# Kernel optimization log

Measured on AMD Instinct MI355X. Metric: run time of the kernel, lower is better.

Reference implementation:

```python
import jax, jax.numpy as jnp
import numpy as np

B, T, N, V, D = 2048, 50, 100, 50000, 512  # batch, targets/ex, noises/ex (=2*T), vocab, label_size


def setup_inputs() -> dict:
    key = jax.random.key(0)
    k1, k2, k3, k4 = jax.random.split(key, 4)
    features = jax.random.normal(k1, (B, D), dtype=jnp.float32)
    targets = jax.random.randint(k2, (B, T), 0, V, dtype=jnp.int64)
    noises = jax.random.randint(k3, (B, N), 0, V, dtype=jnp.int64)
    W = jax.random.normal(k4, (V, D), dtype=jnp.float32) * 0.02  # h2o.weight [V, D]
    return {"features": features, "targets": targets, "noises": noises, "W": W}


def reference(features, targets, noises, W):
    # Per example: out = concat([W[targets] @ f, -(W[noises] @ f)]);
    # loss_i = -mean(logsigmoid(out)); total = sum_i loss_i. (dropout=0 / eval)
    pos = jnp.einsum('btd,bd->bt', W[targets], features)   # [B, T]
    neg = jnp.einsum('bnd,bd->bn', W[noises], features)    # [B, N]
    ls = jax.nn.log_sigmoid
    per_ex = -(jnp.sum(ls(pos), axis=1) + jnp.sum(ls(-neg), axis=1)) / (T + N)
    return jnp.sum(per_ex)
```

## Files before the change

kernel.cpp:

```cpp
#include <hip/hip_runtime.h>
#include <math.h>

constexpr int B_ = 2048;
constexpr int T_ = 50;
constexpr int N_ = 100;
constexpr int D_ = 512;
constexpr int NTOT = T_ + N_;

__global__ __launch_bounds__(256, 8) void nsl_kernel(
    const float* __restrict__ features,
    const int* __restrict__ targets,
    const int* __restrict__ noises,
    const float* __restrict__ W,
    float* __restrict__ out)
{
    const int b    = blockIdx.x;
    const int tid  = threadIdx.x;
    const int lane = tid & 63;
    const int wave = tid >> 6;

    __shared__ int   s_idx[NTOT];
    __shared__ float s_wsum[4];

    if (tid < T_)          s_idx[tid] = targets[(size_t)b * T_ + tid];
    else if (tid < NTOT)   s_idx[tid] = noises[(size_t)b * N_ + (tid - T_)];
    __syncthreads();

    const float4* f4 = reinterpret_cast<const float4*>(features + (size_t)b * D_);
    const float4 fa = f4[lane];
    const float4 fb = f4[lane + 64];

    float acc = 0.f;

    for (int t = wave; t < NTOT; t += 4) {
        const int idx = s_idx[t];
        const float4* w4 = reinterpret_cast<const float4*>(W + (size_t)idx * D_);
        const float4 wa = w4[lane];
        const float4 wb = w4[lane + 64];

        float p = wa.x * fa.x + wa.y * fa.y + wa.z * fa.z + wa.w * fa.w
                + wb.x * fb.x + wb.y * fb.y + wb.z * fb.z + wb.w * fb.w;

        #pragma unroll
        for (int s = 32; s >= 1; s >>= 1)
            p += __shfl_xor(p, s, 64);

        const float x = (t < T_) ? p : -p;
        const float ls = fminf(x, 0.f) - log1pf(__expf(-fabsf(x)));
        acc += ls;
    }

    if (lane == 0) s_wsum[wave] = acc;
    __syncthreads();

    if (tid == 0) {
        const float s = s_wsum[0] + s_wsum[1] + s_wsum[2] + s_wsum[3];
        atomicAdd(out, -s / (float)NTOT);
    }
}

extern "C" void kernel_launch(void* const* d_in, const int* in_sizes, int n_in,
                              void* d_out, int out_size, void* d_ws, size_t ws_size,
                              hipStream_t stream) {
    const float* features = (const float*)d_in[0];
    const int*   targets  = (const int*)d_in[1];
    const int*   noises   = (const int*)d_in[2];
    const float* W        = (const float*)d_in[3];
    float*       out      = (float*)d_out;

    hipMemsetAsync(out, 0, sizeof(float), stream);

    nsl_kernel<<<B_, 256, 0, stream>>>(features, targets, noises, W, out);
}
```

Before: 226.8 us.

## Gather eight rows per wave iteration with transposed butterfly shuffle reduction

Each wave now issues loads for eight gathered W rows per iteration instead of one, which keeps more memory requests in flight for this bandwidth-bound gather. The per-row full wave reductions are replaced by a transposed butterfly that reduces eight partial dot products together, cutting shuffle count. Each result ends up replicated across eight lanes, so the final sum is divided by eight to compensate. The index list is padded to 152 entries, and the padded rows load row 0 and are masked out. The log1p call is replaced by the faster __logf, which gives up a little accuracy. Holding eight rows at once raises register pressure.

Result: no change. 224.1 us (-1.2%).

```diff
diff --git a/kernel.cpp b/kernel.cpp
--- a/kernel.cpp
+++ b/kernel.cpp
@@ -1,11 +1,13 @@
 #include <hip/hip_runtime.h>
 #include <math.h>
 
-constexpr int B_ = 2048;
-constexpr int T_ = 50;
-constexpr int N_ = 100;
-constexpr int D_ = 512;
+constexpr int B_   = 2048;
+constexpr int T_   = 50;
+constexpr int N_   = 100;
+constexpr int D_   = 512;
 constexpr int NTOT = T_ + N_;
+constexpr int NPAD = 152;
+constexpr int NCHK = NPAD / 8;
 
 __global__ __launch_bounds__(256, 8) void nsl_kernel(
     const float* __restrict__ features,
@@ -19,11 +21,12 @@
     const int lane = tid & 63;
     const int wave = tid >> 6;
 
-    __shared__ int   s_idx[NTOT];
+    __shared__ int   s_idx[NPAD];
     __shared__ float s_wsum[4];
 
     if (tid < T_)          s_idx[tid] = targets[(size_t)b * T_ + tid];
     else if (tid < NTOT)   s_idx[tid] = noises[(size_t)b * N_ + (tid - T_)];
+    else if (tid < NPAD)   s_idx[tid] = 0;
     __syncthreads();
 
     const float4* f4 = reinterpret_cast<const float4*>(features + (size_t)b * D_);
@@ -32,30 +35,59 @@
 
     float acc = 0.f;
 
-    for (int t = wave; t < NTOT; t += 4) {
-        const int idx = s_idx[t];
-        const float4* w4 = reinterpret_cast<const float4*>(W + (size_t)idx * D_);
-        const float4 wa = w4[lane];
-        const float4 wb = w4[lane + 64];
-
-        float p = wa.x * fa.x + wa.y * fa.y + wa.z * fa.z + wa.w * fa.w
-                + wb.x * fb.x + wb.y * fb.y + wb.z * fb.z + wb.w * fb.w;
+    for (int k = wave; k < NCHK; k += 4) {
+        float p[8];
+        #pragma unroll
+        for (int j = 0; j < 8; ++j) {
+            const int idx = s_idx[8 * k + j];
+            const float4* w4 = reinterpret_cast<const float4*>(W + (size_t)idx * D_);
+            const float4 wa = w4[lane];
+            const float4 wb = w4[lane + 64];
+            p[j] = wa.x * fa.x + wa.y * fa.y + wa.z * fa.z + wa.w * fa.w
+                 + wb.x * fb.x + wb.y * fb.y + wb.z * fb.z + wb.w * fb.w;
+        }
 
         #pragma unroll
-        for (int s = 32; s >= 1; s >>= 1)
-            p += __shfl_xor(p, s, 64);
+        for (int j = 0; j < 4; ++j) {
+            const float a = p[2 * j], c = p[2 * j + 1];
+            const float own = (lane & 1) ? c : a;
+            const float oth = (lane & 1) ? a : c;
+            p[j] = own + __shfl_xor(oth, 1, 64);
+        }
+        #pragma unroll
+        for (int j = 0; j < 2; ++j) {
+            const float a = p[2 * j], c = p[2 * j + 1];
+            const float own = (lane & 2) ? c : a;
+            const float oth = (lane & 2) ? a : c;
+            p[j] = own + __shfl_xor(oth, 2, 64);
+        }
+        {
+            const float a = p[0], c = p[1];
+            const float own = (lane & 4) ? c : a;
+            const float oth = (lane & 4) ? a : c;
+            p[0] = own + __shfl_xor(oth, 4, 64);
+        }
+        float q = p[0];
+        q += __shfl_xor(q, 8, 64);
+        q += __shfl_xor(q, 16, 64);
+        q += __shfl_xor(q, 32, 64);
 
-        const float x = (t < T_) ? p : -p;
-        const float ls = fminf(x, 0.f) - log1pf(__expf(-fabsf(x)));
-        acc += ls;
+        const int r = 8 * k + (lane & 7);
+        const float x  = (r < T_) ? q : -q;
+        const float ls = fminf(x, 0.f) - __logf(1.f + __expf(-fabsf(x)));
+        if (r < NTOT) acc += ls;
     }
+
+    #pragma unroll
+    for (int s = 32; s >= 1; s >>= 1)
+        acc += __shfl_xor(acc, s, 64);
 
     if (lane == 0) s_wsum[wave] = acc;
     __syncthreads();
 
     if (tid == 0) {
         const float s = s_wsum[0] + s_wsum[1] + s_wsum[2] + s_wsum[3];
-        atomicAdd(out, -s / (float)NTOT);
+        atomicAdd(out, -s / (8.0f * (float)NTOT));
     }
 }
 
```
